# Performance work log

Measured on AMD Instinct MI355X. Metric: run time of the kernel, lower is better.

The kernel has to match this reference:

```python
import jax, jax.numpy as jnp
import numpy as np
import itertools

DIM = 7
N_H2, N_H3 = 21, 77

def _perm_sign(p):
    inv = sum(1 for i in range(len(p)) for j in range(i + 1, len(p)) if p[i] > p[j])
    return -1.0 if inv % 2 else 1.0

def _build_wedge_constants():
    # C[a,b,c] = sign of (pair_a, pair_b, triple_c) as a permutation of (0..6),
    # zero unless the 2+2+3 indices are disjoint (coefficient of the volume form
    # in omega_a ^ omega_b ^ Phi_c on ordered-multi-index components).
    idx2 = list(itertools.combinations(range(DIM), 2))   # 21 ordered pairs
    idx3 = list(itertools.combinations(range(DIM), 3))   # 35 ordered triples
    C = np.zeros((len(idx2), len(idx2), len(idx3)), dtype=np.float32)
    for a, pa in enumerate(idx2):
        sa = set(pa)
        for b, pb in enumerate(idx2):
            if sa & set(pb):
                continue
            sab = sa | set(pb)
            for c, pc in enumerate(idx3):
                full = pa + pb + pc
                if sab.isdisjoint(pc):
                    C[a, b, c] = _perm_sign(full)
    return jnp.asarray(C)

C_WEDGE = _build_wedge_constants()  # (21, 21, 35), sparse structure constants

def setup_inputs() -> dict:
    key = jax.random.key(0)
    k1, k2, k3 = jax.random.split(key, 3)
    batch = 4096
    omega = jax.random.normal(k1, (batch, N_H2, 21), dtype=jnp.float32)
    Phi = jax.random.normal(k2, (batch, N_H3, 35), dtype=jnp.float32)
    metric = jax.random.normal(k3, (batch, DIM, DIM), dtype=jnp.float32)
    return {"omega": omega, "Phi": Phi, "metric": metric}

def reference(omega, Phi, metric):
    # Monte-Carlo volume weights, normalized (normalize=True path)
    vol = jnp.sqrt(jnp.abs(jnp.linalg.det(metric)))        # (n,)
    w = vol / vol.sum()
    # Fused triple wedge contraction replacing the 21*21*77 python loops:
    # D[n,i,j,c] = sum_{a,b} C[a,b,c] omega[n,i,a] omega[n,j,b]
    D = jnp.einsum('abc,nia,njb->nijc', C_WEDGE, omega, omega)
    Pw = Phi * w[:, None, None]                             # fold MC weight into Phi
    S = jnp.einsum('nijc,nkc->ijk', D, Pw)                  # (21,21,77), symmetric in i,j
    # Original code writes +integral for j>=i and forces -integral for j<i
    upper = jnp.triu(jnp.ones((N_H2, N_H2), dtype=bool))[:, :, None]
    Y = jnp.where(upper, S, -S)
    # Gram matrix and spectrum
    M = jnp.einsum('ijk,ijl->kl', Y, Y)                     # (77,77)
    eigenvalues = jnp.linalg.eigvalsh(M)[::-1]              # descending, like torch path
    return Y, M, eigenvalues
```

## Files before the change

### kernel.cpp

```cpp
#include <hip/hip_runtime.h>
#include <math.h>

#define NBATCH 4096
#define NH2 21
#define NK 77
#define NC 35
#define NIJ 441
#define Y_SIZE 33957
#define M_SIZE 5929
#define VOLOFF Y_SIZE
#define VSUM (Y_SIZE + 4096)
#define NPAIR 231
#define BLK 512
#define NPB 8
#define GRID_B (NBATCH / NPB)
#define EIGT 640

#define NSLOT 16
#define SLOT_STRIDE 17792
#define WS2OFF (NSLOT * SLOT_STRIDE)

#define SZ_OMEGA  (NBATCH * NH2 * NH2)
#define SZ_PHI    (NBATCH * NK * NC)
#define SZ_METRIC (NBATCH * 7 * 7)

struct WTab {
  int a[NC][6];
  int b[NC][6];
  int sg[NC][6];
};

constexpr WTab make_wtab() {
  WTab W{};
  int p0[21] = {}, p1[21] = {};
  int idx = 0;
  for (int x = 0; x < 7; ++x)
    for (int y = x + 1; y < 7; ++y) { p0[idx] = x; p1[idx] = y; ++idx; }
  int t0[35] = {}, t1[35] = {}, t2[35] = {};
  idx = 0;
  for (int x = 0; x < 7; ++x)
    for (int y = x + 1; y < 7; ++y)
      for (int z = y + 1; z < 7; ++z) { t0[idx] = x; t1[idx] = y; t2[idx] = z; ++idx; }
  int cnt[35] = {};
  for (int a = 0; a < 21; ++a)
    for (int b = 0; b < 21; ++b) {
      int pa0 = p0[a], pa1 = p1[a], pb0 = p0[b], pb1 = p1[b];
      if (pa0 == pb0 || pa0 == pb1 || pa1 == pb0 || pa1 == pb1) continue;
      bool used[7] = {};
      used[pa0] = true; used[pa1] = true; used[pb0] = true; used[pb1] = true;
      int tr[3] = {}; int k = 0;
      for (int x = 0; x < 7; ++x) if (!used[x]) tr[k++] = x;
      int c = -1;
      for (int cc = 0; cc < 35; ++cc)
        if (t0[cc] == tr[0] && t1[cc] == tr[1] && t2[cc] == tr[2]) { c = cc; break; }
      int perm[7] = {pa0, pa1, pb0, pb1, tr[0], tr[1], tr[2]};
      int inv = 0;
      for (int i = 0; i < 7; ++i)
        for (int j = i + 1; j < 7; ++j)
          if (perm[i] > perm[j]) ++inv;
      W.a[c][cnt[c]] = a; W.b[c][cnt[c]] = b; W.sg[c][cnt[c]] = (inv & 1) ? -1 : 1;
      ++cnt[c];
    }
  return W;
}

__device__ __forceinline__ int trioff(int i) { return 21 * i - (i * (i - 1)) / 2; }

__device__ __forceinline__ unsigned f2bf(float x) {
  union { float f; unsigned u; } v; v.f = x;
  return ((v.u + 0x7FFFu + ((v.u >> 16) & 1u)) >> 16) & 0xFFFFu;
}

typedef float f32x4 __attribute__((ext_vector_type(4)));
typedef float f32x2 __attribute__((ext_vector_type(2)));
typedef short s16x8 __attribute__((ext_vector_type(8)));

__device__ __forceinline__ f32x2 pk_fma(f32x2 a, f32x2 b, f32x2 c) {
  f32x2 d;
  asm("v_pk_fma_f32 %0, %1, %2, %3" : "=v"(d) : "v"(a), "v"(b), "v"(c));
  return d;
}

template <int CTRL>
__device__ __forceinline__ float dppadd(float x) {
  union { float f; int i; } u, r;
  u.f = x;
  r.i = __builtin_amdgcn_update_dpp(0, u.i, CTRL, 0xF, 0xF, true);
  return x + r.f;
}
__device__ __forceinline__ float oct_sum(float x) {
  x = dppadd<0xB1>(x);
  x = dppadd<0x4E>(x);
  x = dppadd<0x141>(x);
  return x;
}
__device__ __forceinline__ float wave_sum(float x) {
  x = dppadd<0xB1>(x);
  x = dppadd<0x4E>(x);
  x = dppadd<0x141>(x);
  x = dppadd<0x140>(x);
  x = dppadd<0x142>(x);
  x = dppadd<0x143>(x);
  return x;
}
__device__ __forceinline__ float readlane63(float x) {
  union { float f; int i; } u; u.f = x;
  union { int i; float f; } r;
  r.i = __builtin_amdgcn_readlane(u.i, 63);
  return r.f;
}
__device__ __forceinline__ float readlane0(float x) {
  union { float f; int i; } u; u.f = x;
  union { int i; float f; } r;
  r.i = __builtin_amdgcn_readfirstlane(u.i);
  return r.f;
}
__device__ __forceinline__ float readlaneN(float x, int lane) {
  union { float f; int i; } u; u.f = x;
  union { int i; float f; } r;
  r.i = __builtin_amdgcn_readlane(u.i, lane);
  return r.f;
}

__global__ __launch_bounds__(256) void vol_kernel(const float* __restrict__ metric,
                                                  float* __restrict__ out) {
  const int n = blockIdx.x * 256 + threadIdx.x;
  double a[7][7];
#pragma unroll
  for (int r = 0; r < 7; ++r)
#pragma unroll
    for (int c = 0; c < 7; ++c) a[r][c] = (double)metric[n * 49 + r * 7 + c];

  double det = 1.0;
#pragma unroll
  for (int k = 0; k < 7; ++k) {
#pragma unroll
    for (int r = k + 1; r < 7; ++r) {
      bool sw = fabs(a[r][k]) > fabs(a[k][k]);
#pragma unroll
      for (int c = k; c < 7; ++c) {
        double u = a[k][c], v = a[r][c];
        a[k][c] = sw ? v : u;
        a[r][c] = sw ? u : v;
      }
    }
    det *= a[k][k];
    double inv = (a[k][k] != 0.0) ? 1.0 / a[k][k] : 0.0;
#pragma unroll
    for (int r = k + 1; r < 7; ++r) {
      double f = a[r][k] * inv;
#pragma unroll
      for (int c = k + 1; c < 7; ++c) a[r][c] -= f * a[k][c];
    }
  }
  float vol = (float)sqrt(fabs(det));
  out[VOLOFF + n] = vol;

  float s = vol;
#pragma unroll
  for (int off = 32; off > 0; off >>= 1) s += __shfl_down(s, off, 64);
  __shared__ float partial[4];
  const int lane = threadIdx.x & 63, wv = threadIdx.x >> 6;
  if (lane == 0) partial[wv] = s;
  __syncthreads();
  if (threadIdx.x == 0)
    atomicAdd(out + VSUM, partial[0] + partial[1] + partial[2] + partial[3]);
}

__global__ __launch_bounds__(BLK) void contract_kernel(const float* __restrict__ omega,
                                                       const float* __restrict__ Phi,
                                                       const float* __restrict__ out,
                                                       float* __restrict__ wsS) {
  constexpr WTab W = make_wtab();
  __shared__ __align__(16) short ldsD[256 * 80];
  __shared__ __align__(16) short ldsP[80 * 80];
  __shared__ __align__(16) float ldsO[NH2 * 28];

  const int t = threadIdx.x;
  const int lane = t & 63;
  const int wv = t >> 6;
  const int quad = lane >> 4;
  const int col = lane & 15;
  const int n0 = blockIdx.x * NPB;

  for (int f = t; f < 256 * 40; f += BLK) ((int*)ldsD)[f] = 0;
  for (int f = t; f < 80 * 40; f += BLK) ((int*)ldsP)[f] = 0;

  const bool roleA = (t < NPAIR);
  const bool roleB = (t >= 256) && (t < 256 + NPAIR);
  int pi = 0, pj = 0;
  {
    const int p = roleA ? t : (roleB ? (t - 256) : 0);
    int i = 0;
    while (i < 20 && trioff(i + 1) <= p) ++i;
    pi = i;
    pj = p - trioff(i) + i;
  }

  float rA = 0.0f, rB[6], rvn;
  {
    const float* om = omega + n0 * 441;
    const float* ph = Phi + n0 * 2695;
    if (t < 441) rA = om[t];
#pragma unroll
    for (int j = 0; j < 6; ++j) {
      const int e = t + j * BLK;
      rB[j] = (e < 2695) ? ph[e] : 0.0f;
    }
    rvn = out[VOLOFF + n0];
  }

  f32x4 acc[2][5];
#pragma unroll
  for (int mi = 0; mi < 2; ++mi)
#pragma unroll
    for (int nt = 0; nt < 5; ++nt) acc[mi][nt] = (f32x4){0.f, 0.f, 0.f, 0.f};

  for (int it = 0; it < NPB; ++it) {
    __syncthreads();

    if (t < 441) ldsO[(t / 21) * 28 + (t % 21)] = rA;
    {
      const float vn = rvn;
#pragma unroll
      for (int j = 0; j < 6; ++j) {
        const int e = t + j * BLK;
        if (e < 2695) {
          const int q = e / 35, c = e % 35;
          ldsP[q * 80 + c] = (short)f2bf(vn * rB[j]);
        }
      }
    }
    __syncthreads();

    if (it + 1 < NPB) {
      const int n1 = n0 + it + 1;
      const float* om2 = omega + n1 * 441;
      const float* ph2 = Phi + n1 * 2695;
      if (t < 441) rA = om2[t];
#pragma unroll
      for (int j = 0; j < 6; ++j) {
        const int e = t + j * BLK;
        if (e < 2695) rB[j] = ph2[e];
      }
      rvn = out[VOLOFF + n1];
    }

    if (roleA || roleB) {
      float wi[21], wj[21];
      const float* oi = ldsO + pi * 28;
      const float* oj = ldsO + pj * 28;
#pragma unroll
      for (int a = 0; a < 20; a += 4) {
        float4 v = *(const float4*)(oi + a);
        wi[a] = v.x; wi[a + 1] = v.y; wi[a + 2] = v.z; wi[a + 3] = v.w;
        float4 u = *(const float4*)(oj + a);
        wj[a] = u.x; wj[a + 1] = u.y; wj[a + 2] = u.z; wj[a + 3] = u.w;
      }
      wi[20] = oi[20]; wj[20] = oj[20];

      if (roleA) {
        float d[18];
#pragma unroll
        for (int c = 0; c < 18; ++c) {
          float dd = 0.0f;
#pragma unroll
          for (int u = 0; u < 6; ++u)
            dd = fmaf((W.sg[c][u] > 0) ? wi[W.a[c][u]] : -wi[W.a[c][u]], wj[W.b[c][u]], dd);
          d[c] = dd;
        }
        int* Drow = (int*)ldsD + t * 40;
#pragma unroll
        for (int k2 = 0; k2 < 9; ++k2)
          Drow[k2] = (int)(f2bf(d[2 * k2]) | (f2bf(d[2 * k2 + 1]) << 16));
      } else {
        float d[17];
#pragma unroll
        for (int c = 18; c < 35; ++c) {
          float dd = 0.0f;
#pragma unroll
          for (int u = 0; u < 6; ++u)
            dd = fmaf((W.sg[c][u] > 0) ? wi[W.a[c][u]] : -wi[W.a[c][u]], wj[W.b[c][u]], dd);
          d[c - 18] = dd;
        }
        int* Drow = (int*)ldsD + (t - 256) * 40;
#pragma unroll
        for (int k2 = 0; k2 < 8; ++k2)
          Drow[9 + k2] = (int)(f2bf(d[2 * k2]) | (f2bf(d[2 * k2 + 1]) << 16));
        Drow[17] = (int)f2bf(d[16]);
      }
    }
    __syncthreads();

#pragma unroll
    for (int s = 0; s < 2; ++s) {
      const int kof = s * 32 + quad * 8;
      s16x8 a0 = *(const s16x8*)(ldsD + ((wv * 2 + 0) * 16 + col) * 80 + kof);
      s16x8 a1 = *(const s16x8*)(ldsD + ((wv * 2 + 1) * 16 + col) * 80 + kof);
      s16x8 b[5];
#pragma unroll
      for (int nt = 0; nt < 5; ++nt)
        b[nt] = *(const s16x8*)(ldsP + (nt * 16 + col) * 80 + kof);
#pragma unroll
      for (int nt = 0; nt < 5; ++nt) {
        acc[0][nt] = __builtin_amdgcn_mfma_f32_16x16x32_bf16(a0, b[nt], acc[0][nt], 0, 0, 0);
        acc[1][nt] = __builtin_amdgcn_mfma_f32_16x16x32_bf16(a1, b[nt], acc[1][nt], 0, 0, 0);
      }
    }
  }

  float* slot = wsS + (size_t)(blockIdx.x & (NSLOT - 1)) * SLOT_STRIDE;
#pragma unroll
  for (int mi = 0; mi < 2; ++mi) {
    const int mt = wv * 2 + mi;
#pragma unroll
    for (int r = 0; r < 4; ++r) {
      const int m = mt * 16 + quad * 4 + r;
      if (m < NPAIR) {
#pragma unroll
        for (int nt = 0; nt < 5; ++nt) {
          const int q = nt * 16 + col;
          if (q < 77) atomicAdd(&slot[m * NK + q], acc[mi][nt][r]);
        }
      }
    }
  }
}

__global__ __launch_bounds__(256) void finalize_y(const float* __restrict__ wsS,
                                                  float* __restrict__ out) {
  const int e = blockIdx.x * 256 + threadIdx.x;
  if (e >= NPAIR * NK) return;
  const int p = e / NK, k = e % NK;
  int i = 0;
  while (i < 20 && trioff(i + 1) <= p) ++i;
  const int j = p - trioff(i) + i;
  float v = 0.0f;
#pragma unroll
  for (int s = 0; s < NSLOT; ++s) v += wsS[(size_t)s * SLOT_STRIDE + p * NK + k];
  v *= 1.0f / out[VSUM];
  out[(i * 21 + j) * NK + k] = v;
  if (j != i) out[(j * 21 + i) * NK + k] = -v;
}

__global__ __launch_bounds__(EIGT) void gram_kernel(const float* __restrict__ Y,
                                                    float* __restrict__ Mout) {
  const int k = blockIdx.x;
  const int t = threadIdx.x;
  const int l = t >> 3, s = t & 7;
  float acc = 0.0f;
  if (l < NK) {
    for (int ij = s; ij < NIJ; ij += 8)
      acc = fmaf(Y[ij * NK + k], Y[ij * NK + l], acc);
  }
  acc = oct_sum(acc);
  if (s == 0 && l < NK) Mout[k * NK + l] = acc;
}

__global__ __launch_bounds__(64, 1) void tridiag_kernel(const float* __restrict__ Min,
                                                        float* __restrict__ ws2) {
  const int l = threadIdx.x;
  const int br = l >> 3, bc = l & 7;
  f32x2 A2[10][5];
#pragma unroll
  for (int r = 0; r < 10; ++r) {
    const int g = 10 * br + r;
#pragma unroll
    for (int c2 = 0; c2 < 5; ++c2) {
      const int gc0 = 10 * bc + 2 * c2;
      A2[r][c2][0] = (g < 77 && gc0 < 77) ? Min[g * 77 + gc0] : 0.0f;
      A2[r][c2][1] = (g < 77 && gc0 + 1 < 77) ? Min[g * 77 + gc0 + 1] : 0.0f;
    }
  }

  float rc[10], rr[10];
#pragma unroll
  for (int c2 = 0; c2 < 5; ++c2) {
    rc[2 * c2]     = __shfl(A2[0][c2][0], bc, 64);
    rc[2 * c2 + 1] = __shfl(A2[0][c2][1], bc, 64);
    rr[2 * c2]     = __shfl(A2[0][c2][0], br, 64);
    rr[2 * c2 + 1] = __shfl(A2[0][c2][1], br, 64);
  }

#pragma unroll 1
  for (int kb = 0; kb < 8; ++kb) {
#pragma unroll
    for (int ko = 0; ko < 10; ++ko) {
      if (kb == 7 && ko >= 5) break;
      const int k = kb * 10 + ko;
      const int nko = (ko + 1) % 10;
      const int nkb = kb + (ko == 9 ? 1 : 0);
      const int nic = nkb * 8 + bc, nir = nkb * 8 + br;

      float part = 0.0f;
      if (br == 0) {
#pragma unroll
        for (int c2 = 0; c2 < 5; ++c2) {
          const int gc0 = 10 * bc + 2 * c2;
          const float x0 = rc[2 * c2], xv = rc[2 * c2 + 1];
          part += (gc0 > k) ? x0 * x0 : 0.0f;
          part += (gc0 + 1 > k) ? xv * xv : 0.0f;
        }
      }
      part = oct_sum(part);
      const float sigma2 = readlane0(part);
      if (sigma2 < 1e-26f) {
        if (l == 0) ws2[80 + k] = 0.0f;
#pragma unroll
        for (int c2 = 0; c2 < 5; ++c2) {
          rc[2 * c2]     = __shfl(A2[nko][c2][0], nic, 64);
          rc[2 * c2 + 1] = __shfl(A2[nko][c2][1], nic, 64);
          rr[2 * c2]     = __shfl(A2[nko][c2][0], nir, 64);
          rr[2 * c2 + 1] = __shfl(A2[nko][c2][1], nir, 64);
        }
        continue;
      }
      const float x1 = readlaneN(rc[nko], nkb);
      const float sigma = __builtin_amdgcn_sqrtf(sigma2);
      const float alpha = (x1 >= 0.0f) ? -sigma : sigma;
      const float beta = __builtin_amdgcn_rcpf(fmaf(-alpha, x1, sigma2));
      const float xha = x1 - alpha;
      if (l == 0) ws2[80 + k] = alpha;

      f32x2 vc2[5];
      float vr[10];
#pragma unroll
      for (int c2 = 0; c2 < 5; ++c2) {
        const int gc0 = 10 * bc + 2 * c2;
        vc2[c2][0] = (gc0 > k) ? ((gc0 == k + 1) ? xha : rc[2 * c2]) : 0.0f;
        vc2[c2][1] = (gc0 + 1 > k) ? ((gc0 + 1 == k + 1) ? xha : rc[2 * c2 + 1]) : 0.0f;
        const int gr0 = 10 * br + 2 * c2;
        vr[2 * c2] = (gr0 > k) ? ((gr0 == k + 1) ? xha : rr[2 * c2]) : 0.0f;
        vr[2 * c2 + 1] = (gr0 + 1 > k) ? ((gr0 + 1 == k + 1) ? xha : rr[2 * c2 + 1]) : 0.0f;
      }

      float p[10];
#pragma unroll
      for (int r = 0; r < 10; ++r) {
        f32x2 a = (f32x2){0.f, 0.f};
#pragma unroll
        for (int c2 = 0; c2 < 5; ++c2) a = pk_fma(A2[r][c2], vc2[c2], a);
        p[r] = a[0] + a[1];
      }
#pragma unroll
      for (int r = 0; r < 10; ++r) {
        p[r] = oct_sum(p[r]) * beta;
        p[r] = (10 * br + r > k) ? p[r] : 0.0f;
      }

      f32x2 pc2[5];
#pragma unroll
      for (int c2 = 0; c2 < 5; ++c2) {
        pc2[c2][0] = __shfl(p[2 * c2], 9 * bc, 64);
        pc2[c2][1] = __shfl(p[2 * c2 + 1], 9 * bc, 64);
      }

      float kp = 0.0f;
      if (bc == 0) {
#pragma unroll
        for (int r = 0; r < 10; ++r) kp = fmaf(p[r], vr[r], kp);
      }
      kp = wave_sum(kp);
      const float hb = 0.5f * beta * readlane63(kp);

      float w[10];
#pragma unroll
      for (int r = 0; r < 10; ++r) w[r] = fmaf(-hb, vr[r], p[r]);
      const f32x2 mhb = (f32x2){-hb, -hb};
      f32x2 wc2[5];
#pragma unroll
      for (int c2 = 0; c2 < 5; ++c2) wc2[c2] = pk_fma(mhb, vc2[c2], pc2[c2]);

      {
        const f32x2 nv = (f32x2){-vr[nko], -vr[nko]};
        const f32x2 nw = (f32x2){-w[nko], -w[nko]};
#pragma unroll
        for (int c2 = 0; c2 < 5; ++c2)
          A2[nko][c2] = pk_fma(nv, wc2[c2], pk_fma(nw, vc2[c2], A2[nko][c2]));
      }
#pragma unroll
      for (int c2 = 0; c2 < 5; ++c2) {
        rc[2 * c2]     = __shfl(A2[nko][c2][0], nic, 64);
        rc[2 * c2 + 1] = __shfl(A2[nko][c2][1], nic, 64);
        rr[2 * c2]     = __shfl(A2[nko][c2][0], nir, 64);
        rr[2 * c2 + 1] = __shfl(A2[nko][c2][1], nir, 64);
      }
#pragma unroll
      for (int r = 0; r < 10; ++r) {
        if (r == nko) continue;
        const f32x2 nv = (f32x2){-vr[r], -vr[r]};
        const f32x2 nw = (f32x2){-w[r], -w[r]};
#pragma unroll
        for (int c2 = 0; c2 < 5; ++c2)
          A2[r][c2] = pk_fma(nv, wc2[c2], pk_fma(nw, vc2[c2], A2[r][c2]));
      }
    }
  }

  if (br == bc) {
#pragma unroll
    for (int e = 0; e < 10; ++e)
      ws2[10 * br + e] = (e & 1) ? A2[e][e / 2][1] : A2[e][e / 2][0];
  }
  if (l == 63) ws2[80 + 75] = A2[6][2][1];
}

__global__ __launch_bounds__(EIGT) void bisect_kernel(const float* __restrict__ ws2,
                                                      float* __restrict__ eout) {
  __shared__ float dsh[80], esh[80], e2sh[80];
  __shared__ float red[10], red2[10];
  const int t = threadIdx.x;
  const int lane = t & 63, wv = t >> 6;
  if (t < 80) {
    dsh[t] = ws2[t];
    esh[t] = (t < 76) ? ws2[80 + t] : 0.0f;
  }
  __syncthreads();
  if (t < 76) e2sh[t] = esh[t] * esh[t];

  float lo_ = 1e30f, hi_ = -1e30f;
  if (t < 77) {
    const float r = ((t > 0) ? fabsf(esh[t - 1]) : 0.0f) +
                    ((t < 76) ? fabsf(esh[t]) : 0.0f);
    lo_ = dsh[t] - r;
    hi_ = dsh[t] + r;
  }
#pragma unroll
  for (int off = 1; off < 64; off <<= 1) {
    lo_ = fminf(lo_, __shfl_xor(lo_, off, 64));
    hi_ = fmaxf(hi_, __shfl_xor(hi_, off, 64));
  }
  if (lane == 0) { red[wv] = lo_; red2[wv] = hi_; }
  __syncthreads();
  lo_ = red[0]; hi_ = red2[0];
#pragma unroll
  for (int u = 1; u < 10; ++u) { lo_ = fminf(lo_, red[u]); hi_ = fmaxf(hi_, red2[u]); }
  const float span = hi_ - lo_;
  const float glo = lo_ - 0.001f * span - 1e-6f;
  const float ghi = hi_ + 0.001f * span + 1e-6f;

  {
    const int e = t >> 3;
    const int s = t & 7;
    const int g = (t & 63) >> 3;
    float lo = glo, hi = ghi;
    for (int r = 0; r < 13; ++r) {
      const float step = (hi - lo) * (1.0f / 9.0f);
      const float x = fmaf(step, (float)(s + 1), lo);
      float q = dsh[0] - x;
      int cnt = (q < 0.0f);
#pragma unroll 4
      for (int i = 1; i < 77; ++i) {
        q = (fabsf(q) < 1e-30f) ? -1e-30f : q;
        q = dsh[i] - x - e2sh[i - 1] * __builtin_amdgcn_rcpf(q);
        cnt += (q < 0.0f);
      }
      const unsigned long long mask = __ballot(cnt > e);
      const int b = (int)((mask >> (g * 8)) & 0xFFull);
      const int z = b ? __builtin_ctz(b) : 8;
      const float nlo = fmaf(step, (float)z, lo);
      hi = (z == 8) ? hi : fmaf(step, (float)(z + 1), lo);
      lo = nlo;
    }
    if (s == 0 && e < 77) eout[76 - e] = 0.5f * (lo + hi);
  }
}

extern "C" void kernel_launch(void* const* d_in, const int* in_sizes, int n_in,
                              void* d_out, int out_size, void* d_ws, size_t ws_size,
                              hipStream_t stream) {
  const float* omega  = (const float*)d_in[0];
  const float* Phi    = (const float*)d_in[1];
  const float* metric = (const float*)d_in[2];
  for (int q = 0; q < n_in && q < 3; ++q) {
    if (in_sizes[q] == SZ_OMEGA)       omega  = (const float*)d_in[q];
    else if (in_sizes[q] == SZ_PHI)    Phi    = (const float*)d_in[q];
    else if (in_sizes[q] == SZ_METRIC) metric = (const float*)d_in[q];
  }

  float* out = (float*)d_out;
  float* ws  = (float*)d_ws;

  hipMemsetAsync(d_out, 0, (size_t)out_size * sizeof(float), stream);
  hipMemsetAsync(d_ws, 0, (size_t)WS2OFF * sizeof(float), stream);

  hipLaunchKernelGGL(vol_kernel, dim3(NBATCH / 256), dim3(256), 0, stream, metric, out);
  hipLaunchKernelGGL(contract_kernel, dim3(GRID_B), dim3(BLK), 0, stream,
                     omega, Phi, out, ws);
  hipLaunchKernelGGL(finalize_y, dim3((NPAIR * NK + 255) / 256), dim3(256), 0, stream,
                     ws, out);
  hipLaunchKernelGGL(gram_kernel, dim3(NK), dim3(EIGT), 0, stream,
                     out, out + Y_SIZE);
  hipLaunchKernelGGL(tridiag_kernel, dim3(1), dim3(64), 0, stream,
                     out + Y_SIZE, ws + WS2OFF);
  hipLaunchKernelGGL(bisect_kernel, dim3(1), dim3(EIGT), 0, stream,
                     ws + WS2OFF, out + Y_SIZE + M_SIZE);
}
```

Before: 342.3 us.

## Fuse tridiagonalization and bisection into one kernel and pipeline Householder norm

Merges the single-wave Householder tridiagonalization with the bisection eigenvalue kernel, so diagonal and off-diagonal values pass through shared memory instead of global workspace and one launch is removed. It also computes the next step's column norm, alpha and beta at the end of the current update rather than at the start of the next iteration. This shortens the serial dependency chain. The cost is that 576 threads sit idle during the tridiagonal phase, plus some extra register pressure.

```diff
diff --git a/kernel.cpp b/kernel.cpp
--- a/kernel.cpp
+++ b/kernel.cpp
@@ -357,55 +357,141 @@
   if (s == 0 && l < NK) Mout[k * NK + l] = acc;
 }
 
-__global__ __launch_bounds__(64, 1) void tridiag_kernel(const float* __restrict__ Min,
-                                                        float* __restrict__ ws2) {
-  const int l = threadIdx.x;
-  const int br = l >> 3, bc = l & 7;
-  f32x2 A2[10][5];
-#pragma unroll
-  for (int r = 0; r < 10; ++r) {
-    const int g = 10 * br + r;
+#define PRECOMP(KN, O2, B2)                                                   \
+  do {                                                                        \
+    float pt_ = 0.0f;                                                         \
+    if (br == 0) {                                                            \
+      _Pragma("unroll") for (int c2_ = 0; c2_ < 5; ++c2_) {                   \
+        const int gc0_ = 10 * bc + 2 * c2_;                                   \
+        const float x0_ = rc[2 * c2_], xv_ = rc[2 * c2_ + 1];                 \
+        pt_ += (gc0_ > (KN)) ? x0_ * x0_ : 0.0f;                              \
+        pt_ += (gc0_ + 1 > (KN)) ? xv_ * xv_ : 0.0f;                          \
+      }                                                                       \
+    }                                                                         \
+    pt_ = oct_sum(pt_);                                                       \
+    sig2c = readlane0(pt_);                                                   \
+    const float x1n_ = readlaneN(rc[(O2)], (B2));                             \
+    const float sg_ = __builtin_amdgcn_sqrtf(sig2c);                          \
+    alpha_c = (x1n_ >= 0.0f) ? -sg_ : sg_;                                    \
+    beta_c = __builtin_amdgcn_rcpf(fmaf(-alpha_c, x1n_, sig2c));              \
+    xha_c = x1n_ - alpha_c;                                                   \
+  } while (0)
+
+__global__ __launch_bounds__(EIGT, 1) void eig_kernel(const float* __restrict__ Min,
+                                                      float* __restrict__ eout) {
+  __shared__ float dsh[80], esh[80], e2sh[80];
+  __shared__ float red[10], red2[10];
+  const int t = threadIdx.x;
+
+  if (t < 64) {
+    const int l = t;
+    const int br = l >> 3, bc = l & 7;
+    f32x2 A2[10][5];
+#pragma unroll
+    for (int r = 0; r < 10; ++r) {
+      const int g = 10 * br + r;
+#pragma unroll
+      for (int c2 = 0; c2 < 5; ++c2) {
+        const int gc0 = 10 * bc + 2 * c2;
+        A2[r][c2][0] = (g < 77 && gc0 < 77) ? Min[g * 77 + gc0] : 0.0f;
+        A2[r][c2][1] = (g < 77 && gc0 + 1 < 77) ? Min[g * 77 + gc0 + 1] : 0.0f;
+      }
+    }
+
+    float rc[10], rr[10];
 #pragma unroll
     for (int c2 = 0; c2 < 5; ++c2) {
-      const int gc0 = 10 * bc + 2 * c2;
-      A2[r][c2][0] = (g < 77 && gc0 < 77) ? Min[g * 77 + gc0] : 0.0f;
-      A2[r][c2][1] = (g < 77 && gc0 + 1 < 77) ? Min[g * 77 + gc0 + 1] : 0.0f;
-    }
-  }
-
-  float rc[10], rr[10];
-#pragma unroll
-  for (int c2 = 0; c2 < 5; ++c2) {
-    rc[2 * c2]     = __shfl(A2[0][c2][0], bc, 64);
-    rc[2 * c2 + 1] = __shfl(A2[0][c2][1], bc, 64);
-    rr[2 * c2]     = __shfl(A2[0][c2][0], br, 64);
-    rr[2 * c2 + 1] = __shfl(A2[0][c2][1], br, 64);
-  }
+      rc[2 * c2]     = __shfl(A2[0][c2][0], bc, 64);
+      rc[2 * c2 + 1] = __shfl(A2[0][c2][1], bc, 64);
+      rr[2 * c2]     = __shfl(A2[0][c2][0], br, 64);
+      rr[2 * c2 + 1] = __shfl(A2[0][c2][1], br, 64);
+    }
+    float sig2c, alpha_c, beta_c, xha_c;
+    PRECOMP(0, 1, 0);
 
 #pragma unroll 1
-  for (int kb = 0; kb < 8; ++kb) {
-#pragma unroll
-    for (int ko = 0; ko < 10; ++ko) {
-      if (kb == 7 && ko >= 5) break;
-      const int k = kb * 10 + ko;
-      const int nko = (ko + 1) % 10;
-      const int nkb = kb + (ko == 9 ? 1 : 0);
-      const int nic = nkb * 8 + bc, nir = nkb * 8 + br;
-
-      float part = 0.0f;
-      if (br == 0) {
+    for (int kb = 0; kb < 8; ++kb) {
+#pragma unroll
+      for (int ko = 0; ko < 10; ++ko) {
+        if (kb == 7 && ko >= 5) break;
+        const int k = kb * 10 + ko;
+        const int nko = (ko + 1) % 10;
+        const int nkb = kb + (ko == 9 ? 1 : 0);
+        const int nic = nkb * 8 + bc, nir = nkb * 8 + br;
+        const int o2 = (ko + 2) % 10;
+        const int b2 = kb + (ko + 2) / 10;
+
+        if (sig2c < 1e-26f) {
+          if (l == 0) esh[k] = 0.0f;
+#pragma unroll
+          for (int c2 = 0; c2 < 5; ++c2) {
+            rc[2 * c2]     = __shfl(A2[nko][c2][0], nic, 64);
+            rc[2 * c2 + 1] = __shfl(A2[nko][c2][1], nic, 64);
+            rr[2 * c2]     = __shfl(A2[nko][c2][0], nir, 64);
+            rr[2 * c2 + 1] = __shfl(A2[nko][c2][1], nir, 64);
+          }
+          PRECOMP(k + 1, o2, b2);
+          continue;
+        }
+        const float beta = beta_c, xha = xha_c;
+        if (l == 0) esh[k] = alpha_c;
+
+        f32x2 vc2[5];
+        float vr[10];
 #pragma unroll
         for (int c2 = 0; c2 < 5; ++c2) {
           const int gc0 = 10 * bc + 2 * c2;
-          const float x0 = rc[2 * c2], xv = rc[2 * c2 + 1];
-          part += (gc0 > k) ? x0 * x0 : 0.0f;
-          part += (gc0 + 1 > k) ? xv * xv : 0.0f;
-        }
-      }
-      part = oct_sum(part);
-      const float sigma2 = readlane0(part);
-      if (sigma2 < 1e-26f) {
-        if (l == 0) ws2[80 + k] = 0.0f;
+          vc2[c2][0] = (gc0 > k) ? ((gc0 == k + 1) ? xha : rc[2 * c2]) : 0.0f;
+          vc2[c2][1] = (gc0 + 1 > k) ? ((gc0 + 1 == k + 1) ? xha : rc[2 * c2 + 1]) : 0.0f;
+          const int gr0 = 10 * br + 2 * c2;
+          vr[2 * c2] = (gr0 > k) ? ((gr0 == k + 1) ? xha : rr[2 * c2]) : 0.0f;
+          vr[2 * c2 + 1] = (gr0 + 1 > k) ? ((gr0 + 1 == k + 1) ? xha : rr[2 * c2 + 1]) : 0.0f;
+        }
+
+        float p[10];
+#pragma unroll
+        for (int r = 0; r < 10; ++r) {
+          f32x2 a = (f32x2){0.f, 0.f};
+#pragma unroll
+          for (int c2 = 0; c2 < 5; ++c2) a = pk_fma(A2[r][c2], vc2[c2], a);
+          p[r] = a[0] + a[1];
+        }
+#pragma unroll
+        for (int r = 0; r < 10; ++r) {
+          p[r] = oct_sum(p[r]) * beta;
+          p[r] = (10 * br + r > k) ? p[r] : 0.0f;
+        }
+
+        f32x2 pc2[5];
+#pragma unroll
+        for (int c2 = 0; c2 < 5; ++c2) {
+          pc2[c2][0] = __shfl(p[2 * c2], 9 * bc, 64);
+          pc2[c2][1] = __shfl(p[2 * c2 + 1], 9 * bc, 64);
+        }
+
+        float kp = 0.0f;
+        if (bc == 0) {
+#pragma unroll
+          for (int r = 0; r < 10; ++r) kp = fmaf(p[r], vr[r], kp);
+        }
+        kp = wave_sum(kp);
+        const float hb = 0.5f * beta * readlane63(kp);
+
+        float w[10];
+#pragma unroll
+        for (int r = 0; r < 10; ++r) w[r] = fmaf(-hb, vr[r], p[r]);
+        const f32x2 mhb = (f32x2){-hb, -hb};
+        f32x2 wc2[5];
+#pragma unroll
+        for (int c2 = 0; c2 < 5; ++c2) wc2[c2] = pk_fma(mhb, vc2[c2], pc2[c2]);
+
+        {
+          const f32x2 nv = (f32x2){-vr[nko], -vr[nko]};
+          const f32x2 nw = (f32x2){-w[nko], -w[nko]};
+#pragma unroll
+          for (int c2 = 0; c2 < 5; ++c2)
+            A2[nko][c2] = pk_fma(nv, wc2[c2], pk_fma(nw, vc2[c2], A2[nko][c2]));
+        }
 #pragma unroll
         for (int c2 = 0; c2 < 5; ++c2) {
           rc[2 * c2]     = __shfl(A2[nko][c2][0], nic, 64);
@@ -413,109 +499,30 @@
           rr[2 * c2]     = __shfl(A2[nko][c2][0], nir, 64);
           rr[2 * c2 + 1] = __shfl(A2[nko][c2][1], nir, 64);
         }
-        continue;
-      }
-      const float x1 = readlaneN(rc[nko], nkb);
-      const float sigma = __builtin_amdgcn_sqrtf(sigma2);
-      const float alpha = (x1 >= 0.0f) ? -sigma : sigma;
-      const float beta = __builtin_amdgcn_rcpf(fmaf(-alpha, x1, sigma2));
-      const float xha = x1 - alpha;
-      if (l == 0) ws2[80 + k] = alpha;
-
-      f32x2 vc2[5];
-      float vr[10];
-#pragma unroll
-      for (int c2 = 0; c2 < 5; ++c2) {
-        const int gc0 = 10 * bc + 2 * c2;
-        vc2[c2][0] = (gc0 > k) ? ((gc0 == k + 1) ? xha : rc[2 * c2]) : 0.0f;
-        vc2[c2][1] = (gc0 + 1 > k) ? ((gc0 + 1 == k + 1) ? xha : rc[2 * c2 + 1]) : 0.0f;
-        const int gr0 = 10 * br + 2 * c2;
-        vr[2 * c2] = (gr0 > k) ? ((gr0 == k + 1) ? xha : rr[2 * c2]) : 0.0f;
-        vr[2 * c2 + 1] = (gr0 + 1 > k) ? ((gr0 + 1 == k + 1) ? xha : rr[2 * c2 + 1]) : 0.0f;
-      }
-
-      float p[10];
-#pragma unroll
-      for (int r = 0; r < 10; ++r) {
-        f32x2 a = (f32x2){0.f, 0.f};
-#pragma unroll
-        for (int c2 = 0; c2 < 5; ++c2) a = pk_fma(A2[r][c2], vc2[c2], a);
-        p[r] = a[0] + a[1];
-      }
-#pragma unroll
-      for (int r = 0; r < 10; ++r) {
-        p[r] = oct_sum(p[r]) * beta;
-        p[r] = (10 * br + r > k) ? p[r] : 0.0f;
-      }
-
-      f32x2 pc2[5];
-#pragma unroll
-      for (int c2 = 0; c2 < 5; ++c2) {
-        pc2[c2][0] = __shfl(p[2 * c2], 9 * bc, 64);
-        pc2[c2][1] = __shfl(p[2 * c2 + 1], 9 * bc, 64);
-      }
-
-      float kp = 0.0f;
-      if (bc == 0) {
-#pragma unroll
-        for (int r = 0; r < 10; ++r) kp = fmaf(p[r], vr[r], kp);
-      }
-      kp = wave_sum(kp);
-      const float hb = 0.5f * beta * readlane63(kp);
-
-      float w[10];
-#pragma unroll
-      for (int r = 0; r < 10; ++r) w[r] = fmaf(-hb, vr[r], p[r]);
-      const f32x2 mhb = (f32x2){-hb, -hb};
-      f32x2 wc2[5];
-#pragma unroll
-      for (int c2 = 0; c2 < 5; ++c2) wc2[c2] = pk_fma(mhb, vc2[c2], pc2[c2]);
-
-      {
-        const f32x2 nv = (f32x2){-vr[nko], -vr[nko]};
-        const f32x2 nw = (f32x2){-w[nko], -w[nko]};
-#pragma unroll
-        for (int c2 = 0; c2 < 5; ++c2)
-          A2[nko][c2] = pk_fma(nv, wc2[c2], pk_fma(nw, vc2[c2], A2[nko][c2]));
-      }
-#pragma unroll
-      for (int c2 = 0; c2 < 5; ++c2) {
-        rc[2 * c2]     = __shfl(A2[nko][c2][0], nic, 64);
-        rc[2 * c2 + 1] = __shfl(A2[nko][c2][1], nic, 64);
-        rr[2 * c2]     = __shfl(A2[nko][c2][0], nir, 64);
-        rr[2 * c2 + 1] = __shfl(A2[nko][c2][1], nir, 64);
-      }
-#pragma unroll
-      for (int r = 0; r < 10; ++r) {
-        if (r == nko) continue;
-        const f32x2 nv = (f32x2){-vr[r], -vr[r]};
-        const f32x2 nw = (f32x2){-w[r], -w[r]};
-#pragma unroll
-        for (int c2 = 0; c2 < 5; ++c2)
-          A2[r][c2] = pk_fma(nv, wc2[c2], pk_fma(nw, vc2[c2], A2[r][c2]));
-      }
-    }
-  }
-
-  if (br == bc) {
-#pragma unroll
-    for (int e = 0; e < 10; ++e)
-      ws2[10 * br + e] = (e & 1) ? A2[e][e / 2][1] : A2[e][e / 2][0];
-  }
-  if (l == 63) ws2[80 + 75] = A2[6][2][1];
-}
-
-__global__ __launch_bounds__(EIGT) void bisect_kernel(const float* __restrict__ ws2,
-                                                      float* __restrict__ eout) {
-  __shared__ float dsh[80], esh[80], e2sh[80];
-  __shared__ float red[10], red2[10];
-  const int t = threadIdx.x;
+#pragma unroll
+        for (int r = 0; r < 10; ++r) {
+          if (r == nko) continue;
+          const f32x2 nv = (f32x2){-vr[r], -vr[r]};
+          const f32x2 nw = (f32x2){-w[r], -w[r]};
+#pragma unroll
+          for (int c2 = 0; c2 < 5; ++c2)
+            A2[r][c2] = pk_fma(nv, wc2[c2], pk_fma(nw, vc2[c2], A2[r][c2]));
+        }
+
+        PRECOMP(k + 1, o2, b2);
+      }
+    }
+
+    if (br == bc) {
+#pragma unroll
+      for (int e = 0; e < 10; ++e)
+        dsh[10 * br + e] = (e & 1) ? A2[e][e / 2][1] : A2[e][e / 2][0];
+    }
+    if (l == 63) esh[75] = A2[6][2][1];
+  }
+  __syncthreads();
+
   const int lane = t & 63, wv = t >> 6;
-  if (t < 80) {
-    dsh[t] = ws2[t];
-    esh[t] = (t < 76) ? ws2[80 + t] : 0.0f;
-  }
-  __syncthreads();
   if (t < 76) e2sh[t] = esh[t] * esh[t];
 
   float lo_ = 1e30f, hi_ = -1e30f;
@@ -591,8 +598,6 @@
                      ws, out);
   hipLaunchKernelGGL(gram_kernel, dim3(NK), dim3(EIGT), 0, stream,
                      out, out + Y_SIZE);
-  hipLaunchKernelGGL(tridiag_kernel, dim3(1), dim3(64), 0, stream,
-                     out + Y_SIZE, ws + WS2OFF);
-  hipLaunchKernelGGL(bisect_kernel, dim3(1), dim3(EIGT), 0, stream,
-                     ws + WS2OFF, out + Y_SIZE + M_SIZE);
-}
+  hipLaunchKernelGGL(eig_kernel, dim3(1), dim3(EIGT), 0, stream,
+                     out + Y_SIZE, out + Y_SIZE + M_SIZE);
+}
```

Measured after the change: 557.9 us. +63.0%, slower.
